# Kernel tuning notes

Measured on AMD Instinct MI355X. Metric: run time of the kernel, lower is better.

The kernel has to match this reference:

```python
import jax, jax.numpy as jnp
import numpy as np

DIM = 2048
CTX_DIM = 1024
N_HEADS = 32
HEAD_DIM = DIM // N_HEADS  # 64
POS_DIM = 2
B, N, CTXN = 2, 2048, 2048
ROPE_BASE = 10000.0


def apply_axial_rope(x, pos):
    # x: (B, N, H, D), pos: (B, N, P). Split D across the P position axes,
    # rotate consecutive pairs within each axis chunk by angle pos_p * freq.
    b, n, h, d = x.shape
    p = pos.shape[-1]
    dpa = d // p           # dims per axis
    half = dpa // 2        # rotation pairs per axis
    freqs = ROPE_BASE ** (-jnp.arange(half, dtype=x.dtype) / half)  # (half,)
    ang = pos[..., :, None] * freqs            # (B, N, P, half)
    cos = jnp.cos(ang)[:, :, None, :, :]       # (B, N, 1, P, half)
    sin = jnp.sin(ang)[:, :, None, :, :]
    xr = x.reshape(b, n, h, p, half, 2)
    x1, x2 = xr[..., 0], xr[..., 1]
    out = jnp.stack([x1 * cos - x2 * sin, x1 * sin + x2 * cos], axis=-1)
    return out.reshape(b, n, h, d)


def setup_inputs() -> dict:
    key = jax.random.key(0)
    ks = jax.random.split(key, 8)
    x = jax.random.normal(ks[0], (B, N, DIM), jnp.float32)
    ctx = jax.random.normal(ks[1], (B, CTXN, CTX_DIM), jnp.float32)
    pos_map = jax.random.uniform(ks[2], (B, N, POS_DIM), jnp.float32)
    ctx_pos_map = jax.random.uniform(ks[3], (B, CTXN, POS_DIM), jnp.float32)
    # flax Linear kernels: (in_features, out_features), lecun_normal-ish scale
    Wq = jax.random.normal(ks[4], (DIM, DIM), jnp.float32) / np.sqrt(DIM)
    Wkv = jax.random.normal(ks[5], (CTX_DIM, 2 * DIM), jnp.float32) / np.sqrt(CTX_DIM)
    Wout = jax.random.normal(ks[6], (DIM, DIM), jnp.float32) / np.sqrt(DIM)
    bout = jnp.zeros((DIM,), jnp.float32)
    return {"x": x, "ctx": ctx, "pos_map": pos_map, "ctx_pos_map": ctx_pos_map,
            "Wq": Wq, "Wkv": Wkv, "Wout": Wout, "bout": bout}


def reference(x, ctx, pos_map, ctx_pos_map, Wq, Wkv, Wout, bout):
    b, n, _ = x.shape
    ctx_n = ctx.shape[1]
    q = (x @ Wq).reshape(b, n, N_HEADS, HEAD_DIM)
    k, v = jnp.split(ctx @ Wkv, 2, axis=-1)
    k = k.reshape(b, ctx_n, N_HEADS, HEAD_DIM)
    v = v.reshape(b, ctx_n, N_HEADS, HEAD_DIM)
    q = apply_axial_rope(q, pos_map)
    k = apply_axial_rope(k, ctx_pos_map)
    # scaled dot-product attention (flax dot_product_attention, mask=None)
    scale = 1.0 / np.sqrt(HEAD_DIM).astype(np.float32)
    logits = jnp.einsum("bqhd,bkhd->bhqk", q, k) * scale
    w = jax.nn.softmax(logits, axis=-1)
    attn = jnp.einsum("bhqk,bkhd->bqhd", w, v)
    attn = attn.reshape(b, n, N_HEADS * HEAD_DIM)
    return attn @ Wout + bout
```

## Files before the change

kernel.cpp:

```cpp
#include <hip/hip_runtime.h>
#include <hip/hip_bf16.h>

#define NH 32
#define HD 64
#define DMODEL 2048
#define CTXD 1024
#define NB 2
#define NSEQ 2048
#define NCTX 2048

typedef __attribute__((ext_vector_type(8))) short bf16x8;
typedef __attribute__((ext_vector_type(4))) float f32x4;
typedef __attribute__((ext_vector_type(4))) short s16x4;
typedef __attribute__((ext_vector_type(2))) float f32x2;
typedef __attribute__((ext_vector_type(4))) unsigned int u32x4;

__device__ __forceinline__ unsigned short f2b(float f) {
  unsigned int u = __builtin_bit_cast(unsigned int, f);
  u = u + 0x7fffu + ((u >> 16) & 1u);
  return (unsigned short)(u >> 16);
}

__device__ __forceinline__ unsigned int cvtpk(float lo, float hi) {
  unsigned int r;
  asm("v_cvt_pk_bf16_f32 %0, %1, %2" : "=v"(r) : "v"(lo), "v"(hi));
  return r;
}

__device__ __forceinline__ float exp2a(float x) {
  float r;
  asm("v_exp_f32 %0, %1" : "=v"(r) : "v"(x));
  return r;
}

__device__ __forceinline__ void async16(const void* g, void* l) {
  __builtin_amdgcn_global_load_lds((const __attribute__((address_space(1))) void*)g,
                                   (__attribute__((address_space(3))) void*)l, 16, 0, 0);
}

__global__ void k_cast2(const float* __restrict__ x, const float* __restrict__ ctx,
                        unsigned short* __restrict__ xbf, unsigned short* __restrict__ ctxbf) {
  int i = blockIdx.x * blockDim.x + threadIdx.x;
  const float* in = x;
  unsigned short* out = xbf;
  if (i >= 2097152) {
    in = ctx;
    out = ctxbf;
    i -= 2097152;
  }
  float4 v = ((const float4*)in)[i];
  s16x4 o;
  o.x = (short)f2b(v.x);
  o.y = (short)f2b(v.y);
  o.z = (short)f2b(v.z);
  o.w = (short)f2b(v.w);
  ((s16x4*)out)[i] = o;
}

__global__ void k_tcast3(const float* __restrict__ Wq, const float* __restrict__ Wkv,
                         const float* __restrict__ Wout, unsigned short* __restrict__ wqt,
                         unsigned short* __restrict__ wkvt, unsigned short* __restrict__ woutt) {
  __shared__ float t[32][33];
  const int z = blockIdx.z;
  const float* in;
  unsigned short* out;
  int R, C;
  if (z == 0) {
    if (blockIdx.x >= 64) return;
    in = Wq; out = wqt; R = 2048; C = 2048;
  } else if (z == 1) {
    if (blockIdx.y >= 32) return;
    in = Wkv; out = wkvt; R = 1024; C = 4096;
  } else {
    if (blockIdx.x >= 64) return;
    in = Wout; out = woutt; R = 2048; C = 2048;
  }
  const int tx = threadIdx.x, ty = threadIdx.y;
  const int c0 = blockIdx.x * 32, r0 = blockIdx.y * 32;
#pragma unroll
  for (int j = 0; j < 4; j++)
    t[ty + j * 8][tx] = in[(size_t)(r0 + ty + j * 8) * C + c0 + tx];
  __syncthreads();
#pragma unroll
  for (int j = 0; j < 4; j++)
    out[(size_t)(c0 + ty + j * 8) * R + r0 + tx] = f2b(t[tx][ty + j * 8]);
}

__global__ void k_ropetab2(const float* __restrict__ pos, const float* __restrict__ cpos,
                           f32x2* __restrict__ csq, f32x2* __restrict__ csk) {
  int gidx = blockIdx.x * blockDim.x + threadIdx.x;
  const float* p = pos;
  f32x2* cs = csq;
  int idx = gidx;
  if (gidx >= 131072) {
    p = cpos;
    cs = csk;
    idx = gidx - 131072;
  }
  int i = idx & 15;
  int pp = (idx >> 4) & 1;
  int bn = idx >> 5;
  float freq = powf(10000.0f, -(float)i / 16.0f);
  float ang = p[bn * 2 + pp] * freq;
  float s, c;
  sincosf(ang, &s, &c);
  f32x2 r;
  r.x = c;
  r.y = s;
  cs[idx] = r;
}

template <int EPI, int BK>
__launch_bounds__(256) __global__
void k_gemm(const unsigned short* __restrict__ A, const unsigned short* __restrict__ BT,
            unsigned short* __restrict__ out0, unsigned short* __restrict__ out1,
            float* __restrict__ foutp, const f32x2* __restrict__ cs,
            const float* __restrict__ bias, int K) {
  constexpr int CPR = BK / 8;
  constexpr int RPT = (128 * CPR) / 256;
  constexpr int KS = BK / 32;
  __shared__ __align__(1024) unsigned short As[2][128 * BK];
  __shared__ __align__(1024) unsigned short Bs[2][128 * BK];
  const int tid = threadIdx.x;
  const int wave = tid >> 6, lane = tid & 63;
  const int g = lane >> 4, lr = lane & 15;
  const int bm = blockIdx.y * 128, bn = blockIdx.x * 128;
  const int wr = wave >> 1, wc = wave & 1;

  f32x4 acc[4][4];
#pragma unroll
  for (int m = 0; m < 4; m++)
#pragma unroll
    for (int n = 0; n < 4; n++) acc[m][n] = (f32x4){0.f, 0.f, 0.f, 0.f};

  auto stage = [&](int bi, int kt) {
#pragma unroll
    for (int r = 0; r < RPT; ++r) {
      const int cid = tid + r * 256;
      const int row = cid / CPR, ch = cid % CPR;
      const int chs = (BK == 64) ? (ch ^ (row & 7)) : ch;
      async16(A + (size_t)(bm + row) * K + kt + chs * 8, &As[bi][cid * 8]);
      async16(BT + (size_t)(bn + row) * K + kt + chs * 8, &Bs[bi][cid * 8]);
    }
  };

  stage(0, 0);
  __syncthreads();
  int cur = 0;
  const int NT = K / BK;

  for (int t = 0; t < NT; ++t) {
    if (t < NT - 1) stage(cur ^ 1, (t + 1) * BK);
    bf16x8 af[4][KS], bfr[4][KS];
#pragma unroll
    for (int m = 0; m < 4; m++) {
      const int ra = wr * 64 + m * 16 + lr;
      const int rb = wc * 64 + m * 16 + lr;
#pragma unroll
      for (int ks = 0; ks < KS; ks++) {
        const int ca = (BK == 64) ? (((ks << 2) | g) ^ (ra & 7)) : g;
        const int cb = (BK == 64) ? (((ks << 2) | g) ^ (rb & 7)) : g;
        af[m][ks] = *(const bf16x8*)(&As[cur][ra * BK + ca * 8]);
        bfr[m][ks] = *(const bf16x8*)(&Bs[cur][rb * BK + cb * 8]);
      }
    }
    __builtin_amdgcn_s_setprio(1);
#pragma unroll
    for (int ks = 0; ks < KS; ks++)
#pragma unroll
      for (int m = 0; m < 4; m++)
#pragma unroll
        for (int n = 0; n < 4; n++)
          acc[m][n] = __builtin_amdgcn_mfma_f32_16x16x32_bf16(af[m][ks], bfr[n][ks],
                                                              acc[m][n], 0, 0, 0);
    __builtin_amdgcn_s_setprio(0);
    __syncthreads();
    cur ^= 1;
  }

  if constexpr (EPI == 2) {
#pragma unroll
    for (int m = 0; m < 4; m++)
#pragma unroll
      for (int n = 0; n < 4; n++)
#pragma unroll
        for (int r2 = 0; r2 < 4; r2++) {
          int row = bm + wr * 64 + m * 16 + g * 4 + r2;
          int col = bn + wc * 64 + n * 16 + lr;
          foutp[(size_t)row * DMODEL + col] = acc[m][n][r2] + bias[col];
        }
  } else {
    const bool dorope = (EPI == 0) || (bn < DMODEL);
#pragma unroll
    for (int m = 0; m < 4; m++)
#pragma unroll
      for (int n = 0; n < 4; n++)
#pragma unroll
        for (int r2 = 0; r2 < 4; r2++) {
          int row = bm + wr * 64 + m * 16 + g * 4 + r2;
          int col = bn + wc * 64 + n * 16 + lr;
          float v = acc[m][n][r2];
          float pv = __shfl_xor(v, 1);
          int bb = row >> 11, nn = row & (NSEQ - 1);
          if (dorope) {
            int hh = col >> 6, d = col & 63;
            f32x2 sc = cs[((row << 1) + (d >> 5)) * 16 + ((d >> 1) & 15)];
            float o = (d & 1) ? (pv * sc.y + v * sc.x) : (v * sc.x - pv * sc.y);
            if constexpr (EPI == 0) o *= 0.125f * 1.44269504088896f;
            out0[(((size_t)(bb * NH + hh)) * NSEQ + nn) * HD + d] = f2b(o);
          } else {
            int c2 = col - DMODEL;
            int hh = c2 >> 6, d = c2 & 63;
            int tile = nn >> 6, kv = nn & 63;
            int sc2 = ((kv >> 5) << 2) | ((kv >> 2) & 3);
            int cc = sc2 ^ (d & 7);
            int j = (((kv >> 4) & 1) << 2) | (kv & 3);
            out1[(size_t)(bb * NH + hh) * (NCTX * HD) + tile * 4096 + d * 64 + cc * 8 + j] =
                f2b(v);
          }
        }
  }
}

__launch_bounds__(256, 4) __global__
void k_attn(const unsigned short* __restrict__ Q, const unsigned short* __restrict__ K,
            const unsigned short* __restrict__ VT, unsigned short* __restrict__ O) {
  __shared__ __align__(1024) unsigned short Kl[2][64 * 64];
  __shared__ __align__(1024) unsigned short Vl[2][64 * 64];
  const int tid = threadIdx.x;
  const int wave = tid >> 6, lane = tid & 63;
  const int g = lane >> 4, lr = lane & 15;
  const int wid = ((blockIdx.x & 7) << 7) + (blockIdx.x >> 3);
  const int qt = wid & 15, h = (wid >> 4) & 31, b = wid >> 9;
  const int bh = b * NH + h;
  const size_t headoff = (size_t)bh * NSEQ * HD;
  const int q0 = qt * 128 + wave * 32;

  bf16x8 qf[2][2];
#pragma unroll
  for (int qs = 0; qs < 2; qs++)
#pragma unroll
    for (int ks = 0; ks < 2; ks++)
      qf[qs][ks] = *(const bf16x8*)(Q + headoff + (size_t)(q0 + qs * 16 + lr) * HD + ks * 32 + g * 8);

  f32x4 accO[2][4];
#pragma unroll
  for (int qs = 0; qs < 2; qs++)
#pragma unroll
    for (int c = 0; c < 4; c++) accO[qs][c] = (f32x4){0.f, 0.f, 0.f, 0.f};
  f32x4 accL[2] = {(f32x4){0.f, 0.f, 0.f, 0.f}, (f32x4){0.f, 0.f, 0.f, 0.f}};

  const unsigned short c1 = 0x3F80;
  const bf16x8 ones = {(short)c1, (short)c1, (short)c1, (short)c1,
                       (short)c1, (short)c1, (short)c1, (short)c1};

  const int srow = tid >> 3;
  const unsigned short* kSrc = K + headoff + (size_t)srow * HD + (((tid & 7) ^ (srow & 7)) << 3);
  const unsigned short* vSrc = VT + (size_t)bh * (NCTX * HD) + tid * 8;

  auto stage = [&](int bi, int kv0) {
#pragma unroll
    for (int r = 0; r < 2; ++r) {
      async16(kSrc + (size_t)(kv0 + r * 32) * HD, &Kl[bi][(r * 4 + wave) * 512]);
      async16(vSrc + (size_t)kv0 * 64 + r * 2048, &Vl[bi][(r * 4 + wave) * 512]);
    }
  };

  stage(0, 0);
  __syncthreads();
  int cur = 0;

  for (int t = 0; t < NCTX / 64; ++t) {
    if (t < NCTX / 64 - 1) stage(cur ^ 1, (t + 1) * 64);

    const unsigned short* Kc = &Kl[cur][0];
    const unsigned short* Vc = &Vl[cur][0];

    f32x4 s[2][4];
#pragma unroll
    for (int qs = 0; qs < 2; qs++)
#pragma unroll
      for (int sub = 0; sub < 4; sub++) s[qs][sub] = (f32x4){-16.f, -16.f, -16.f, -16.f};
    __builtin_amdgcn_s_setprio(1);
#pragma unroll
    for (int sub = 0; sub < 4; ++sub) {
      const int kvr = sub * 16 + lr;
#pragma unroll
      for (int ks = 0; ks < 2; ++ks) {
        bf16x8 kf = *(const bf16x8*)(Kc + kvr * 64 + (((ks * 4 + g) ^ (kvr & 7)) << 3));
        s[0][sub] = __builtin_amdgcn_mfma_f32_16x16x32_bf16(kf, qf[0][ks], s[0][sub], 0, 0, 0);
        s[1][sub] = __builtin_amdgcn_mfma_f32_16x16x32_bf16(kf, qf[1][ks], s[1][sub], 0, 0, 0);
      }
    }
    __builtin_amdgcn_s_setprio(0);

    bf16x8 pb[2][2];
#pragma unroll
    for (int qs = 0; qs < 2; ++qs) {
#pragma unroll
      for (int sub = 0; sub < 4; sub++)
#pragma unroll
        for (int r2 = 0; r2 < 4; r2++) s[qs][sub][r2] = exp2a(s[qs][sub][r2]);
#pragma unroll
      for (int kg = 0; kg < 2; kg++) {
        u32x4 w;
        w.x = cvtpk(s[qs][2 * kg][0], s[qs][2 * kg][1]);
        w.y = cvtpk(s[qs][2 * kg][2], s[qs][2 * kg][3]);
        w.z = cvtpk(s[qs][2 * kg + 1][0], s[qs][2 * kg + 1][1]);
        w.w = cvtpk(s[qs][2 * kg + 1][2], s[qs][2 * kg + 1][3]);
        pb[qs][kg] = __builtin_bit_cast(bf16x8, w);
      }
    }

    __builtin_amdgcn_s_setprio(1);
#pragma unroll
    for (int c = 0; c < 4; ++c) {
      const int d = c * 16 + lr;
#pragma unroll
      for (int kg = 0; kg < 2; ++kg) {
        bf16x8 vf = *(const bf16x8*)(Vc + d * 64 + ((kg * 32 + g * 8) ^ ((d & 7) << 3)));
        accO[0][c] = __builtin_amdgcn_mfma_f32_16x16x32_bf16(vf, pb[0][kg], accO[0][c], 0, 0, 0);
        accO[1][c] = __builtin_amdgcn_mfma_f32_16x16x32_bf16(vf, pb[1][kg], accO[1][c], 0, 0, 0);
      }
    }
    accL[0] = __builtin_amdgcn_mfma_f32_16x16x32_bf16(ones, pb[0][0], accL[0], 0, 0, 0);
    accL[0] = __builtin_amdgcn_mfma_f32_16x16x32_bf16(ones, pb[0][1], accL[0], 0, 0, 0);
    accL[1] = __builtin_amdgcn_mfma_f32_16x16x32_bf16(ones, pb[1][0], accL[1], 0, 0, 0);
    accL[1] = __builtin_amdgcn_mfma_f32_16x16x32_bf16(ones, pb[1][1], accL[1], 0, 0, 0);
    __builtin_amdgcn_s_setprio(0);
    __syncthreads();
    cur ^= 1;
  }

  const size_t obase = (size_t)b * NSEQ * DMODEL + (size_t)h * HD;
#pragma unroll
  for (int qs = 0; qs < 2; ++qs) {
    float inv = 1.0f / accL[qs][0];
    const int q = q0 + qs * 16 + lr;
#pragma unroll
    for (int c = 0; c < 4; ++c) {
      s16x4 o4;
#pragma unroll
      for (int r2 = 0; r2 < 4; r2++) o4[r2] = (short)f2b(accO[qs][c][r2] * inv);
      *(s16x4*)(O + obase + (size_t)q * DMODEL + c * 16 + 4 * g) = o4;
    }
  }
}

extern "C" void kernel_launch(void* const* d_in, const int* in_sizes, int n_in,
                              void* d_out, int out_size, void* d_ws, size_t ws_size,
                              hipStream_t stream) {
  const float* x = (const float*)d_in[0];
  const float* ctx = (const float*)d_in[1];
  const float* pos_map = (const float*)d_in[2];
  const float* ctx_pos = (const float*)d_in[3];
  const float* Wq = (const float*)d_in[4];
  const float* Wkv = (const float*)d_in[5];
  const float* Wout = (const float*)d_in[6];
  const float* bout = (const float*)d_in[7];
  float* outp = (float*)d_out;

  char* ws = (char*)d_ws;
  unsigned short* xbf = (unsigned short*)(ws + 0);
  unsigned short* vtbf = (unsigned short*)(ws + 0);
  unsigned short* ctxbf = (unsigned short*)(ws + 16777216);
  unsigned short* wqt = (unsigned short*)(ws + 25165824);
  unsigned short* wkvt = (unsigned short*)(ws + 33554432);
  unsigned short* woutt = (unsigned short*)(ws + 41943040);
  unsigned short* qbf = (unsigned short*)(ws + 50331648);
  unsigned short* kbf = (unsigned short*)(ws + 67108864);
  unsigned short* attnbf = (unsigned short*)(ws + 100663296);
  f32x2* csq = (f32x2*)(ws + 117440512);
  f32x2* csk = (f32x2*)(ws + 118489088);

  k_cast2<<<12288, 256, 0, stream>>>(x, ctx, xbf, ctxbf);
  k_tcast3<<<dim3(128, 64, 3), dim3(32, 8), 0, stream>>>(Wq, Wkv, Wout, wqt, wkvt, woutt);
  k_ropetab2<<<1024, 256, 0, stream>>>(pos_map, ctx_pos, csq, csk);

  k_gemm<0, 64><<<dim3(16, 32), 256, 0, stream>>>(xbf, wqt, qbf, nullptr, nullptr, csq, nullptr, 2048);
  k_gemm<1, 64><<<dim3(32, 32), 256, 0, stream>>>(ctxbf, wkvt, kbf, vtbf, nullptr, csk, nullptr, 1024);
  k_attn<<<1024, 256, 0, stream>>>(qbf, kbf, vtbf, attnbf);
  k_gemm<2, 64><<<dim3(16, 32), 256, 0, stream>>>(attnbf, woutt, nullptr, nullptr, outp, nullptr, bout, 2048);
}
```

Measured before the change: 245.2 us.

## Remap GEMM tiles per XCD, merge preprocessing kernels, compact transpose grid

Flattens the GEMM grids to 1D and decodes block IDs so that each of the 8 XCDs gets a contiguous 8x8 patch of output tiles, aiming to improve L2 reuse of A/B panels on the chiplet layout. It also fuses the bf16 cast and RoPE table kernels into one launch. The transpose-cast grid is compacted so no blocks exit early. The gains are expected from cache locality and fewer launches, at the cost of more complex index math.

```diff
diff --git a/kernel.cpp b/kernel.cpp
--- a/kernel.cpp
+++ b/kernel.cpp
@@ -38,45 +38,84 @@
                                    (__attribute__((address_space(3))) void*)l, 16, 0, 0);
 }
 
-__global__ void k_cast2(const float* __restrict__ x, const float* __restrict__ ctx,
-                        unsigned short* __restrict__ xbf, unsigned short* __restrict__ ctxbf) {
-  int i = blockIdx.x * blockDim.x + threadIdx.x;
-  const float* in = x;
-  unsigned short* out = xbf;
-  if (i >= 2097152) {
-    in = ctx;
-    out = ctxbf;
-    i -= 2097152;
-  }
-  float4 v = ((const float4*)in)[i];
-  s16x4 o;
-  o.x = (short)f2b(v.x);
-  o.y = (short)f2b(v.y);
-  o.z = (short)f2b(v.z);
-  o.w = (short)f2b(v.w);
-  ((s16x4*)out)[i] = o;
+template <int GSEL>
+__device__ __forceinline__ void gdecode(int id, int& bx, int& by) {
+  const int xcd = id & 7, r = id >> 3;
+  if constexpr (GSEL == 0) {
+    const int cx = xcd & 1, cy = xcd >> 1;
+    bx = cx * 8 + (r & 7);
+    by = cy * 8 + (r >> 3);
+  } else {
+    const int cid = xcd + 8 * (r >> 6);
+    const int w = r & 63;
+    bx = (cid & 3) * 8 + (w & 7);
+    by = (cid >> 2) * 8 + (w >> 3);
+  }
+}
+
+__global__ void k_pre(const float* __restrict__ x, const float* __restrict__ ctx,
+                      unsigned short* __restrict__ xbf, unsigned short* __restrict__ ctxbf,
+                      const float* __restrict__ pos, const float* __restrict__ cpos,
+                      f32x2* __restrict__ csq, f32x2* __restrict__ csk) {
+  const int bid = blockIdx.x;
+  if (bid < 12288) {
+    int i = bid * 256 + threadIdx.x;
+    const float* in = x;
+    unsigned short* out = xbf;
+    if (i >= 2097152) {
+      in = ctx;
+      out = ctxbf;
+      i -= 2097152;
+    }
+    float4 v = ((const float4*)in)[i];
+    s16x4 o;
+    o.x = (short)f2b(v.x);
+    o.y = (short)f2b(v.y);
+    o.z = (short)f2b(v.z);
+    o.w = (short)f2b(v.w);
+    ((s16x4*)out)[i] = o;
+  } else {
+    int gidx = (bid - 12288) * 256 + threadIdx.x;
+    const float* p = pos;
+    f32x2* cs = csq;
+    int idx = gidx;
+    if (gidx >= 131072) {
+      p = cpos;
+      cs = csk;
+      idx = gidx - 131072;
+    }
+    int i = idx & 15;
+    int pp = (idx >> 4) & 1;
+    int bn = idx >> 5;
+    float freq = powf(10000.0f, -(float)i / 16.0f);
+    float ang = p[bn * 2 + pp] * freq;
+    float s, c;
+    sincosf(ang, &s, &c);
+    f32x2 r;
+    r.x = c;
+    r.y = s;
+    cs[idx] = r;
+  }
 }
 
 __global__ void k_tcast3(const float* __restrict__ Wq, const float* __restrict__ Wkv,
                          const float* __restrict__ Wout, unsigned short* __restrict__ wqt,
                          unsigned short* __restrict__ wkvt, unsigned short* __restrict__ woutt) {
   __shared__ float t[32][33];
-  const int z = blockIdx.z;
+  const int z = blockIdx.x / 4096;
+  const int w = blockIdx.x % 4096;
   const float* in;
   unsigned short* out;
-  int R, C;
+  int R, C, bx, by;
   if (z == 0) {
-    if (blockIdx.x >= 64) return;
-    in = Wq; out = wqt; R = 2048; C = 2048;
+    in = Wq; out = wqt; R = 2048; C = 2048; bx = w % 64; by = w / 64;
   } else if (z == 1) {
-    if (blockIdx.y >= 32) return;
-    in = Wkv; out = wkvt; R = 1024; C = 4096;
+    in = Wkv; out = wkvt; R = 1024; C = 4096; bx = w % 128; by = w / 128;
   } else {
-    if (blockIdx.x >= 64) return;
-    in = Wout; out = woutt; R = 2048; C = 2048;
+    in = Wout; out = woutt; R = 2048; C = 2048; bx = w % 64; by = w / 64;
   }
   const int tx = threadIdx.x, ty = threadIdx.y;
-  const int c0 = blockIdx.x * 32, r0 = blockIdx.y * 32;
+  const int c0 = bx * 32, r0 = by * 32;
 #pragma unroll
   for (int j = 0; j < 4; j++)
     t[ty + j * 8][tx] = in[(size_t)(r0 + ty + j * 8) * C + c0 + tx];
@@ -86,31 +125,7 @@
     out[(size_t)(c0 + ty + j * 8) * R + r0 + tx] = f2b(t[tx][ty + j * 8]);
 }
 
-__global__ void k_ropetab2(const float* __restrict__ pos, const float* __restrict__ cpos,
-                           f32x2* __restrict__ csq, f32x2* __restrict__ csk) {
-  int gidx = blockIdx.x * blockDim.x + threadIdx.x;
-  const float* p = pos;
-  f32x2* cs = csq;
-  int idx = gidx;
-  if (gidx >= 131072) {
-    p = cpos;
-    cs = csk;
-    idx = gidx - 131072;
-  }
-  int i = idx & 15;
-  int pp = (idx >> 4) & 1;
-  int bn = idx >> 5;
-  float freq = powf(10000.0f, -(float)i / 16.0f);
-  float ang = p[bn * 2 + pp] * freq;
-  float s, c;
-  sincosf(ang, &s, &c);
-  f32x2 r;
-  r.x = c;
-  r.y = s;
-  cs[idx] = r;
-}
-
-template <int EPI, int BK>
+template <int EPI, int BK, int GSEL>
 __launch_bounds__(256) __global__
 void k_gemm(const unsigned short* __restrict__ A, const unsigned short* __restrict__ BT,
             unsigned short* __restrict__ out0, unsigned short* __restrict__ out1,
@@ -124,7 +139,9 @@
   const int tid = threadIdx.x;
   const int wave = tid >> 6, lane = tid & 63;
   const int g = lane >> 4, lr = lane & 15;
-  const int bm = blockIdx.y * 128, bn = blockIdx.x * 128;
+  int bx, by;
+  gdecode<GSEL>(blockIdx.x, bx, by);
+  const int bm = by * 128, bn = bx * 128;
   const int wr = wave >> 1, wc = wave & 1;
 
   f32x4 acc[4][4];
@@ -373,12 +390,11 @@
   f32x2* csq = (f32x2*)(ws + 117440512);
   f32x2* csk = (f32x2*)(ws + 118489088);
 
-  k_cast2<<<12288, 256, 0, stream>>>(x, ctx, xbf, ctxbf);
-  k_tcast3<<<dim3(128, 64, 3), dim3(32, 8), 0, stream>>>(Wq, Wkv, Wout, wqt, wkvt, woutt);
-  k_ropetab2<<<1024, 256, 0, stream>>>(pos_map, ctx_pos, csq, csk);
-
-  k_gemm<0, 64><<<dim3(16, 32), 256, 0, stream>>>(xbf, wqt, qbf, nullptr, nullptr, csq, nullptr, 2048);
-  k_gemm<1, 64><<<dim3(32, 32), 256, 0, stream>>>(ctxbf, wkvt, kbf, vtbf, nullptr, csk, nullptr, 1024);
+  k_pre<<<13312, 256, 0, stream>>>(x, ctx, xbf, ctxbf, pos_map, ctx_pos, csq, csk);
+  k_tcast3<<<12288, dim3(32, 8), 0, stream>>>(Wq, Wkv, Wout, wqt, wkvt, woutt);
+
+  k_gemm<0, 64, 0><<<512, 256, 0, stream>>>(xbf, wqt, qbf, nullptr, nullptr, csq, nullptr, 2048);
+  k_gemm<1, 64, 1><<<1024, 256, 0, stream>>>(ctxbf, wkvt, kbf, vtbf, nullptr, csk, nullptr, 1024);
   k_attn<<<1024, 256, 0, stream>>>(qbf, kbf, vtbf, attnbf);
-  k_gemm<2, 64><<<dim3(16, 32), 256, 0, stream>>>(attnbf, woutt, nullptr, nullptr, outp, nullptr, bout, 2048);
-}
+  k_gemm<2, 64, 0><<<512, 256, 0, stream>>>(attnbf, woutt, nullptr, nullptr, outp, nullptr, bout, 2048);
+}
```

After: 234.5 us. 4.3% less time.
